# Optimization experiments

Measured on AMD Instinct MI355X. Metric: run time of the kernel, lower is better.

## Reference

```python
import jax, jax.numpy as jnp
import numpy as np
from jax.scipy.special import logsumexp

B, T, D = 16, 512, 768
S, H, O = 4, 48, 48
EMISS_W = 0.5  # args.emiss_nn_weight


def setup_inputs() -> dict:
    key = jax.random.key(0)
    ks = jax.random.split(key, 6)
    emb = jax.random.normal(ks[0], (B, T, D), jnp.float32)
    # obs must be valid per-source distributions over n_obs (log is taken)
    obs = jax.nn.softmax(2.0 * jax.random.normal(ks[1], (B, T, S, O), jnp.float32), axis=-1)
    # default prior init: priors = 0.001, priors[0] = 1, param = log(priors)
    p = jnp.full((H,), 0.001, jnp.float32).at[0].set(1.0)
    state_priors = jnp.log(p)
    unnorm_trans = jax.random.normal(ks[2], (H, H), jnp.float32)
    unnorm_emiss = jnp.zeros((S, H, O), jnp.float32)
    # xavier_uniform with relu gain for the per-source emission Linears
    bound = np.sqrt(2.0) * np.sqrt(6.0 / (D + H * O))
    W_emiss = jax.random.uniform(ks[3], (S, H * O, D), jnp.float32, -bound, bound)
    b_emiss = jnp.zeros((S, H * O), jnp.float32)
    seq_lengths = jax.random.randint(ks[4], (B,), T // 2, T + 1).astype(jnp.int32)
    seq_lengths = seq_lengths.at[0].set(T)  # max length == T
    return dict(emb=emb, obs=obs, state_priors=state_priors, unnorm_trans=unnorm_trans,
                unnorm_emiss=unnorm_emiss, W_emiss=W_emiss, b_emiss=b_emiss,
                seq_lengths=seq_lengths)


def _lognorm(x):
    return x - logsumexp(x, axis=-1, keepdims=True)


def reference(emb, obs, state_priors, unnorm_trans, unnorm_emiss, W_emiss, b_emiss, seq_lengths):
    lp = jax.nn.log_softmax(state_priors)                 # [H]
    log_trans = jax.nn.log_softmax(unnorm_trans, axis=-1)  # [H,H] (constant over b,t)
    emiss = jax.nn.softmax(unnorm_emiss, axis=-1)          # [S,H,O]

    # neural emissions: per-source Linear(d_emb -> H*O), softmax over O
    logits = jnp.einsum('btd,sod->btso', emb, W_emiss) + b_emiss  # [B,T,S,H*O]
    nn_emiss = jax.nn.softmax(logits.reshape(B, T, S, H, O), axis=-1)
    # (nn_trans is computed by NeuralModule in the original but discarded)

    log_emiss = jnp.log((1.0 - EMISS_W) * emiss[None, None] + EMISS_W * nn_emiss)  # [B,T,S,H,O]
    # log_matmul over obs axis, then sum over sources -> [B,T,H]
    lep = logsumexp(log_emiss + jnp.log(obs)[:, :, :, None, :], axis=-1).sum(axis=2)

    # forward recursion (normalized each step)
    a0 = _lognorm(lp + lep[:, 0])                          # [B,H]

    def fstep(a_prev, lep_t):
        a = _lognorm(lep_t + logsumexp(a_prev[:, :, None] + log_trans[None], axis=1))
        return a, a

    _, alphas = jax.lax.scan(fstep, a0, jnp.swapaxes(lep[:, 1:], 0, 1))
    log_alpha = jnp.concatenate([a0[:, None], jnp.swapaxes(alphas, 0, 1)], axis=1)  # [B,T,H]

    # backward recursion: beta[t] = logsumexp_j(trans[i,j] + lep[t,j] + beta[t+1,j])
    bT = jnp.zeros((B, H), lep.dtype)

    def bstep(b_next, lep_t):
        b = logsumexp(log_trans[None] + (lep_t + b_next)[:, None, :], axis=2)
        return b, b

    _, betas = jax.lax.scan(bstep, bT, jnp.swapaxes(lep[:, :T - 1], 0, 1), reverse=True)
    log_beta = jnp.concatenate([jnp.swapaxes(betas, 0, 1), bT[:, None]], axis=1)  # [B,T,H]
    # per-example roll by (length - T) along time, as in the original
    log_beta = jax.vmap(lambda b, s: jnp.roll(b, s, axis=0))(log_beta, seq_lengths - T)

    log_gamma = _lognorm(log_alpha + log_beta)             # [B,T,H]

    # xi_t = trans + alpha[t-1] (outer-sum) (lep[t] + beta[t]),  t = 1..T-1
    xi = (log_trans[None, None]
          + log_alpha[:, :-1, :, None]
          + (lep[:, 1:] + log_beta[:, 1:])[:, :, None, :])  # [B,T-1,H,H]
    xi = xi - logsumexp(xi, axis=(-2, -1), keepdims=True)

    log_prior = jnp.mean(jnp.sum(jnp.exp(log_gamma[:, 0]) * lp, axis=-1))

    tran_terms = jnp.sum(jnp.exp(xi) * log_trans[None, None], axis=(-2, -1))  # [B,T-1]
    mask_tr = (jnp.arange(T - 1)[None] < (seq_lengths - 1)[:, None]).astype(lep.dtype)
    log_tran = jnp.mean(jnp.sum(tran_terms * mask_tr, axis=1))

    emis_terms = jnp.sum(jnp.exp(log_gamma) * lep, axis=-1)  # [B,T]
    mask_em = (jnp.arange(T)[None] < seq_lengths[:, None]).astype(lep.dtype)
    log_emis = jnp.mean(jnp.sum(emis_terms * mask_em, axis=1))

    return log_prior + log_tran + log_emis
```

## Files before the change

### kernel.cpp

```cpp
#include <hip/hip_runtime.h>
#include <math.h>

namespace {

constexpr int Bn = 16, Tn = 512, Dn = 768, Sn = 4, Hn = 48, On = 48;
constexpr int Mn = Bn * Tn;
constexpr int Gn = Sn * Hn;
constexpr int Nn = Gn * On;
constexpr float EMISS_W = 0.5f;

constexpr size_t OFF_LP   = 0;
constexpr size_t OFF_LT   = 64;
constexpr size_t OFF_PT   = OFF_LT + Hn*Hn;
constexpr size_t OFF_EM   = OFF_PT + Hn*Hn;
constexpr size_t OFF_LEPP = OFF_EM + (size_t)Sn*Hn*On;
constexpr size_t OFF_LEP  = OFF_LEPP + (size_t)Mn*Gn;
constexpr size_t OFF_LA   = OFF_LEP + (size_t)Mn*Hn;
constexpr size_t OFF_LB   = OFF_LA + (size_t)Mn*Hn;
constexpr size_t OFF_RED  = OFF_LB + (size_t)Mn*Hn;
constexpr size_t FLOATS_END = OFF_RED + (size_t)Mn;

typedef __attribute__((ext_vector_type(8))) short short8;
typedef __attribute__((ext_vector_type(4))) float f32x4;

__device__ inline float waveSum(float v){
#pragma unroll
  for (int o = 32; o; o >>= 1) v += __shfl_xor(v, o);
  return v;
}

__device__ inline unsigned short f2bf(float f){
  unsigned int u = __float_as_uint(f);
  u += 0x7FFFu + ((u >> 16) & 1u);
  return (unsigned short)(u >> 16);
}

__device__ inline void gload_lds16(const void* g, void* l){
  __builtin_amdgcn_global_load_lds(
      (const __attribute__((address_space(1))) void*)g,
      (__attribute__((address_space(3))) void*)l, 16, 0, 0);
}

__global__ void conv_kernel(const float* __restrict__ srcA, unsigned short* __restrict__ dstA,
                            int n4a,
                            const float* __restrict__ srcB, unsigned short* __restrict__ dstB,
                            int n4b){
  int i = blockIdx.x * blockDim.x + threadIdx.x;
  const float* s; unsigned short* d; int k;
  if (i < n4a){ s = srcA; d = dstA; k = i; }
  else { k = i - n4a; if (k >= n4b) return; s = srcB; d = dstB; }
  float4 v = ((const float4*)s)[k];
  ushort4 r;
  r.x = f2bf(v.x); r.y = f2bf(v.y); r.z = f2bf(v.z); r.w = f2bf(v.w);
  ((ushort4*)d)[k] = r;
}

__global__ void prep_kernel(const float* __restrict__ sp, const float* __restrict__ ut,
                            const float* __restrict__ ue, float* __restrict__ ws){
  int tid = threadIdx.x;
  float m = -INFINITY;
  for (int h = 0; h < Hn; ++h) m = fmaxf(m, sp[h]);
  float s = 0.f;
  for (int h = 0; h < Hn; ++h) s += __expf(sp[h] - m);
  float lse = m + __logf(s);
  if (tid < Hn) ws[OFF_LP + tid] = sp[tid] - lse;
  if (tid < Hn){
    const float* row = ut + tid * Hn;
    float mm = -INFINITY;
    for (int j = 0; j < Hn; ++j) mm = fmaxf(mm, row[j]);
    float ss = 0.f;
    for (int j = 0; j < Hn; ++j) ss += __expf(row[j] - mm);
    float l = mm + __logf(ss);
    for (int j = 0; j < Hn; ++j){
      float v = row[j] - l;
      ws[OFF_LT + tid*Hn + j] = v;
      ws[OFF_PT + tid*Hn + j] = __expf(v);
    }
  }
  for (int r = tid; r < Sn*Hn; r += blockDim.x){
    const float* row = ue + (size_t)r * On;
    float mm = -INFINITY;
    for (int o = 0; o < On; ++o) mm = fmaxf(mm, row[o]);
    float ss = 0.f;
    for (int o = 0; o < On; ++o) ss += __expf(row[o] - mm);
    float inv = 1.f/ss;
    for (int o = 0; o < On; ++o) ws[OFF_EM + (size_t)r*On + o] = __expf(row[o]-mm)*inv;
  }
}

constexpr int MT = 128, NT2 = 96, KT = 64;

__global__ __launch_bounds__(256) void gemm_lep_kernel(
    const unsigned short* __restrict__ embB, const unsigned short* __restrict__ WB,
    const float* __restrict__ bm, const float* __restrict__ obs,
    float* __restrict__ ws){
  __shared__ __align__(16) char smem[128*97*4];
  __shared__ float bias_s[96], em_s[96];
  const int tid = threadIdx.x, lane = tid & 63, w = tid >> 6;
  const int m0 = blockIdx.x * MT;
  const int N0 = blockIdx.y * NT2;
  if (tid < 96){
    bias_s[tid] = bm[N0 + tid];
    em_s[tid]   = ws[OFF_EM + N0 + tid];
  }
  const int wm = w & 1, wn = w >> 1;
  const int lm = lane & 15, q = lane >> 4;
  const int key = lm & 7;
  const int srow = lane >> 3, spc = lane & 7;

  f32x4 acc[4][3];
#pragma unroll
  for (int i=0;i<4;++i)
#pragma unroll
    for (int j=0;j<3;++j) acc[i][j] = (f32x4){0.f,0.f,0.f,0.f};

  for (int kc = 0; kc < Dn; kc += KT){
    __syncthreads();
#pragma unroll
    for (int i=0;i<4;++i){
      int idx = w*4 + i;
      int row = idx*8 + srow;
      int lc  = spc ^ (row & 7);
      gload_lds16(embB + (size_t)(m0+row)*Dn + kc + lc*8, smem + idx*1024);
    }
#pragma unroll
    for (int i=0;i<3;++i){
      int idx = w*3 + i;
      int row = idx*8 + srow;
      int lc  = spc ^ (row & 7);
      gload_lds16(WB + (size_t)(N0+row)*Dn + kc + lc*8, smem + 16384 + idx*1024);
    }
    __syncthreads();
#pragma unroll
    for (int s = 0; s < 2; ++s){
      short8 af[4], bf[3];
#pragma unroll
      for (int i=0;i<4;++i){
        int row = wm*64 + i*16 + lm;
        af[i] = *(const short8*)(smem + row*128 + (((s*4+q) ^ key) * 16));
      }
#pragma unroll
      for (int j=0;j<3;++j){
        int row = wn*48 + j*16 + lm;
        bf[j] = *(const short8*)(smem + 16384 + row*128 + (((s*4+q) ^ key) * 16));
      }
#pragma unroll
      for (int i=0;i<4;++i)
#pragma unroll
        for (int j=0;j<3;++j)
          acc[i][j] = __builtin_amdgcn_mfma_f32_16x16x32_bf16(af[i], bf[j], acc[i][j], 0, 0, 0);
    }
  }
  __syncthreads();
  float* C = (float*)smem;
#pragma unroll
  for (int i=0;i<4;++i)
#pragma unroll
    for (int j=0;j<3;++j)
#pragma unroll
      for (int r=0;r<4;++r){
        int mrow = wm*64 + i*16 + q*4 + r;
        int ncol = wn*48 + j*16 + lm;
        C[mrow*97 + ncol] = acc[i][j][r];
      }
  __syncthreads();
  {
    const int row = tid >> 1, half = tid & 1;
    const int m = m0 + row;
    const int g = N0/48 + half;
    const int s2 = g / Hn;
    const float* crow = C + row*97 + half*48;
    const float* ob   = obs + ((size_t)m*Sn + s2)*On;
    const float* bi   = bias_s + half*48;
    const float* em   = em_s + half*48;
    float Z=0.f, pd=0.f, eo=0.f;
#pragma unroll
    for (int o=0;o<On;++o){
      float e = __expf(crow[o] + bi[o]);
      float obv = ob[o];
      Z += e;
      pd = fmaf(e, obv, pd);
      eo = fmaf(em[o], obv, eo);
    }
    float val = __logf((1.f-EMISS_W)*eo + EMISS_W*(pd/Z));
    ws[OFF_LEPP + (size_t)m*Gn + g] = val;
  }
}

__global__ void lep_reduce_kernel(float* __restrict__ ws){
  int x = blockIdx.x * blockDim.x + threadIdx.x;
  if (x < Mn*Hn){
    int m = x / Hn, h = x - m*Hn;
    const size_t base = OFF_LEPP + (size_t)m*Gn + h;
    ws[OFF_LEP + x] = ws[base] + ws[base + Hn] + ws[base + 2*Hn] + ws[base + 3*Hn];
  }
}

constexpr int FBW = 40;
constexpr int FBL = 32;

__global__ __launch_bounds__(64) void fb_kernel(float* __restrict__ ws){
  __shared__ __align__(16) float ldsE[72*48];
  __shared__ __align__(16) float ring[2][64];
  const int lane = threadIdx.x;
  const int c    = blockIdx.x;
  const int b    = blockIdx.y;
  const bool fwd = blockIdx.z == 0;
  const bool act = lane < Hn;
  const int t0 = c*FBL, te = t0 + FBL - 1;

  float pt[Hn];
#pragma unroll
  for (int i = 0; i < Hn; ++i)
    pt[i] = act ? (fwd ? ws[OFF_PT + i*Hn + lane] : ws[OFF_PT + lane*Hn + i]) : 0.f;

  int row_lo, nrows, sA, sZ;
  bool exact;
  if (fwd){
    sA = t0 - FBW;
    exact = (sA < 1);
    row_lo = exact ? 0 : sA;
    if (exact) sA = 1;
    sZ = te;
    nrows = te - row_lo + 1;
  } else {
    int th = te + 1 + FBW;
    exact = (th > 510);
    sA = exact ? 510 : th - 1;
    sZ = t0;
    row_lo = t0;
    nrows = sA - t0 + 1;
  }

  {
    const float4* src = (const float4*)(ws + OFF_LEP + ((size_t)b*Tn + row_lo)*Hn);
    int n4 = nrows * (Hn/4);
    for (int i = lane; i < n4; i += 64){
      float4 v = src[i];
      float4 e;
      e.x = __expf(v.x); e.y = __expf(v.y); e.z = __expf(v.z); e.w = __expf(v.w);
      ((float4*)ldsE)[i] = e;
    }
  }
  __syncthreads();

  if (fwd){
    const size_t laF = OFF_LA + (size_t)b * Tn * Hn;
    float v;
    if (exact){
      v = act ? __expf(ws[OFF_LP + lane]) * ldsE[lane] : 0.f;
      if (c == 0 && act) ws[laF + lane] = v;
    } else {
      v = act ? 1.f : 0.f;
    }
    if (act) ring[0][lane] = v;
    __syncthreads();
    int cur = 0;
    for (int t = sA; t <= sZ; ++t){
      float S = waveSum(v);
      const float* rp = ring[cur];
      float s0=0.f,s1=0.f,s2=0.f,s3=0.f;
#pragma unroll
      for (int i = 0; i < Hn; i += 4){
        float4 a = *(const float4*)(rp + i);
        s0 = fmaf(a.x, pt[i+0], s0); s1 = fmaf(a.y, pt[i+1], s1);
        s2 = fmaf(a.z, pt[i+2], s2); s3 = fmaf(a.w, pt[i+3], s3);
      }
      float sd = (s0+s1)+(s2+s3);
      float e = act ? ldsE[(t - row_lo)*Hn + lane] : 0.f;
      float vn = act ? e * sd * (1.f/S) : 0.f;
      cur ^= 1;
      if (act) ring[cur][lane] = vn;
      __syncthreads();
      if (act && t >= t0) ws[laF + (size_t)t*Hn + lane] = vn;
      v = vn;
    }
  } else {
    const size_t lbF = OFF_LB + (size_t)b * Tn * Hn;
    float v = act ? 1.f : 0.f;
    if (exact && c == (Tn/FBL - 1) && act) ws[lbF + (size_t)(Tn-1)*Hn + lane] = 1.f;
    int cur = 0;
    for (int t = sA; t >= sZ; --t){
      float e = act ? ldsE[(t - row_lo)*Hn + lane] : 0.f;
      float wv = e * v;
      if (act) ring[cur][lane] = wv;
      float S = waveSum(wv);
      __syncthreads();
      const float* rp = ring[cur];
      float s0=0.f,s1=0.f,s2=0.f,s3=0.f;
#pragma unroll
      for (int j = 0; j < Hn; j += 4){
        float4 a = *(const float4*)(rp + j);
        s0 = fmaf(a.x, pt[j+0], s0); s1 = fmaf(a.y, pt[j+1], s1);
        s2 = fmaf(a.z, pt[j+2], s2); s3 = fmaf(a.w, pt[j+3], s3);
      }
      float vn = act ? ((s0+s1)+(s2+s3)) * (1.f/S) : 0.f;
      cur ^= 1;
      if (act && t <= te) ws[lbF + (size_t)t*Hn + lane] = vn;
      v = vn;
    }
  }
}

__global__ __launch_bounds__(256) void gamma_xi_kernel(
    const float* __restrict__ ws_c, float* __restrict__ ws,
    const int* __restrict__ seq_len){
  __shared__ float y_s[Hn], lap_s[Hn];
  __shared__ float red[8];
  const int tid = threadIdx.x;
  const int bid = blockIdx.x;
  const int b = bid >> 9, t = bid & (Tn-1);
  const int len = seq_len[b];
  int tb = t + (Tn - len); if (tb >= Tn) tb -= Tn;
  const size_t bt = (size_t)b*Tn + t;
  if (tid < Hn){
    float lb  = ws_c[OFF_LB + ((size_t)b*Tn + tb)*Hn + tid];
    float lep = ws_c[OFF_LEP + bt*Hn + tid];
    y_s[tid] = __expf(lep) * lb;
    if (t >= 1) lap_s[tid] = ws_c[OFF_LA + (bt-1)*Hn + tid];
  }
  float emis_term = 0.f, prior_term = 0.f;
  if (tid < 64){
    int h = (tid < Hn) ? tid : 0;
    float la  = ws_c[OFF_LA + bt*Hn + h];
    float lb  = ws_c[OFF_LB + ((size_t)b*Tn + tb)*Hn + h];
    float lep = ws_c[OFF_LEP + bt*Hn + h];
    float lp  = ws_c[OFF_LP + h];
    float wgt = (tid < Hn) ? la*lb : 0.f;
    float Z = waveSum(wgt);
    float inv = 1.f / Z;
    emis_term  = waveSum(wgt * lep) * inv;
    prior_term = waveSum(wgt * lp) * inv;
  }
  __syncthreads();
  float tran_term = 0.f;
  if (t >= 1){
    float se = 0.f, st = 0.f;
#pragma unroll
    for (int k=0;k<9;++k){
      int e = tid + k*256;
      int i = e / Hn, j = e - i*Hn;
      float e2 = ws_c[OFF_PT + e] * lap_s[i] * y_s[j];
      se += e2;
      st = fmaf(e2, ws_c[OFF_LT + e], st);
    }
    se = waveSum(se);
    st = waveSum(st);
    const int wid = tid >> 6;
    if ((tid & 63) == 0){ red[wid] = se; red[4+wid] = st; }
    __syncthreads();
    if (tid == 0){
      float SE = red[0]+red[1]+red[2]+red[3];
      float ST = red[4]+red[5]+red[6]+red[7];
      tran_term = ST / SE;
    }
  }
  if (tid == 0){
    float tot = 0.f;
    if (t < len)            tot += emis_term;
    if (t == 0)             tot += prior_term;
    if (t >= 1 && t < len)  tot += tran_term;
    ws[OFF_RED + bid] = tot;
  }
}

__global__ __launch_bounds__(256) void sum_kernel(const float* __restrict__ ws,
                                                  float* __restrict__ out){
  __shared__ float red[4];
  const int tid = threadIdx.x;
  float s = 0.f;
  for (int i = tid; i < Mn; i += 256) s += ws[OFF_RED + i];
  s = waveSum(s);
  if ((tid & 63) == 0) red[tid >> 6] = s;
  __syncthreads();
  if (tid == 0) out[0] = (red[0]+red[1]+red[2]+red[3]) * (1.f / Bn);
}

}

extern "C" void kernel_launch(void* const* d_in, const int* in_sizes, int n_in,
                              void* d_out, int out_size, void* d_ws, size_t ws_size,
                              hipStream_t stream){
  const float* emb = (const float*)d_in[0];
  const float* obs = (const float*)d_in[1];
  const float* sp  = (const float*)d_in[2];
  const float* ut  = (const float*)d_in[3];
  const float* ue  = (const float*)d_in[4];
  const float* Wm  = (const float*)d_in[5];
  const float* bm  = (const float*)d_in[6];
  const int*   sl  = (const int*)d_in[7];
  float* ws  = (float*)d_ws;
  float* out = (float*)d_out;
  (void)in_sizes; (void)n_in; (void)ws_size; (void)out_size;

  unsigned short* embB = (unsigned short*)(ws + FLOATS_END);
  unsigned short* WB   = embB + (size_t)Mn * Dn;

  const int n4a = Mn*Dn/4, n4b = Nn*Dn/4;
  conv_kernel<<<(n4a + n4b + 255)/256, 256, 0, stream>>>(emb, embB, n4a, Wm, WB, n4b);
  prep_kernel<<<1, 256, 0, stream>>>(sp, ut, ue, ws);
  gemm_lep_kernel<<<dim3(Mn/MT, Nn/NT2), 256, 0, stream>>>(embB, WB, bm, obs, ws);
  lep_reduce_kernel<<<(Mn*Hn + 255)/256, 256, 0, stream>>>(ws);
  fb_kernel<<<dim3(Tn/FBL, Bn, 2), 64, 0, stream>>>(ws);
  gamma_xi_kernel<<<Bn*Tn, 256, 0, stream>>>(ws, ws, sl);
  sum_kernel<<<1, 256, 0, stream>>>(ws, out);
}
```

Baseline: 322.0 us.

## Fuse prep into conv, drop lep_reduce and sum kernels, shrink fb chunks

Merges the parameter-prep kernel into the bf16 conversion kernel as an extra block, removes the separate per-source lep reduction by summing the four partial LEPP values inside fb_kernel and gamma_xi_kernel, and replaces the final sum kernel with a last-block atomic counter reduction. It also halves the forward/backward chunk length and shortens the warm-up window, which doubles the fb block count and cuts each block's serial chain. This saves three launches and one intermediate buffer pass. In exchange the LEPP reads are repeated across consumers, and the shorter warm-up window may change numerical accuracy.

```diff
diff --git a/kernel.cpp b/kernel.cpp
--- a/kernel.cpp
+++ b/kernel.cpp
@@ -14,11 +14,11 @@
 constexpr size_t OFF_PT   = OFF_LT + Hn*Hn;
 constexpr size_t OFF_EM   = OFF_PT + Hn*Hn;
 constexpr size_t OFF_LEPP = OFF_EM + (size_t)Sn*Hn*On;
-constexpr size_t OFF_LEP  = OFF_LEPP + (size_t)Mn*Gn;
-constexpr size_t OFF_LA   = OFF_LEP + (size_t)Mn*Hn;
+constexpr size_t OFF_LA   = OFF_LEPP + (size_t)Mn*Gn;
 constexpr size_t OFF_LB   = OFF_LA + (size_t)Mn*Hn;
 constexpr size_t OFF_RED  = OFF_LB + (size_t)Mn*Hn;
-constexpr size_t FLOATS_END = OFF_RED + (size_t)Mn;
+constexpr size_t OFF_CNT  = OFF_RED + (size_t)Mn;
+constexpr size_t FLOATS_END = OFF_CNT + 64;
 
 typedef __attribute__((ext_vector_type(8))) short short8;
 typedef __attribute__((ext_vector_type(4))) float f32x4;
@@ -41,51 +41,54 @@
       (__attribute__((address_space(3))) void*)l, 16, 0, 0);
 }
 
-__global__ void conv_kernel(const float* __restrict__ srcA, unsigned short* __restrict__ dstA,
-                            int n4a,
-                            const float* __restrict__ srcB, unsigned short* __restrict__ dstB,
-                            int n4b){
-  int i = blockIdx.x * blockDim.x + threadIdx.x;
-  const float* s; unsigned short* d; int k;
-  if (i < n4a){ s = srcA; d = dstA; k = i; }
-  else { k = i - n4a; if (k >= n4b) return; s = srcB; d = dstB; }
-  float4 v = ((const float4*)s)[k];
+__global__ void convprep_kernel(const float* __restrict__ srcA, unsigned short* __restrict__ dstA,
+                                int n4a,
+                                const float* __restrict__ srcB, unsigned short* __restrict__ dstB,
+                                int n4b,
+                                const float* __restrict__ sp, const float* __restrict__ ut,
+                                const float* __restrict__ ue, float* __restrict__ ws,
+                                int nconv){
+  const int tid = threadIdx.x;
+  if ((int)blockIdx.x == nconv){
+    if (tid == 0) ((unsigned int*)(ws + OFF_CNT))[0] = 0u;
+    float m = -INFINITY;
+    for (int h = 0; h < Hn; ++h) m = fmaxf(m, sp[h]);
+    float s = 0.f;
+    for (int h = 0; h < Hn; ++h) s += __expf(sp[h] - m);
+    float lse = m + __logf(s);
+    if (tid < Hn) ws[OFF_LP + tid] = sp[tid] - lse;
+    if (tid < Hn){
+      const float* row = ut + tid * Hn;
+      float mm = -INFINITY;
+      for (int j = 0; j < Hn; ++j) mm = fmaxf(mm, row[j]);
+      float ss = 0.f;
+      for (int j = 0; j < Hn; ++j) ss += __expf(row[j] - mm);
+      float l = mm + __logf(ss);
+      for (int j = 0; j < Hn; ++j){
+        float v = row[j] - l;
+        ws[OFF_LT + tid*Hn + j] = v;
+        ws[OFF_PT + tid*Hn + j] = __expf(v);
+      }
+    }
+    for (int r = tid; r < Sn*Hn; r += blockDim.x){
+      const float* row = ue + (size_t)r * On;
+      float mm = -INFINITY;
+      for (int o = 0; o < On; ++o) mm = fmaxf(mm, row[o]);
+      float ss = 0.f;
+      for (int o = 0; o < On; ++o) ss += __expf(row[o] - mm);
+      float inv = 1.f/ss;
+      for (int o = 0; o < On; ++o) ws[OFF_EM + (size_t)r*On + o] = __expf(row[o]-mm)*inv;
+    }
+    return;
+  }
+  int i = blockIdx.x * blockDim.x + tid;
+  const float* s2; unsigned short* d; int k;
+  if (i < n4a){ s2 = srcA; d = dstA; k = i; }
+  else { k = i - n4a; if (k >= n4b) return; s2 = srcB; d = dstB; }
+  float4 v = ((const float4*)s2)[k];
   ushort4 r;
   r.x = f2bf(v.x); r.y = f2bf(v.y); r.z = f2bf(v.z); r.w = f2bf(v.w);
   ((ushort4*)d)[k] = r;
-}
-
-__global__ void prep_kernel(const float* __restrict__ sp, const float* __restrict__ ut,
-                            const float* __restrict__ ue, float* __restrict__ ws){
-  int tid = threadIdx.x;
-  float m = -INFINITY;
-  for (int h = 0; h < Hn; ++h) m = fmaxf(m, sp[h]);
-  float s = 0.f;
-  for (int h = 0; h < Hn; ++h) s += __expf(sp[h] - m);
-  float lse = m + __logf(s);
-  if (tid < Hn) ws[OFF_LP + tid] = sp[tid] - lse;
-  if (tid < Hn){
-    const float* row = ut + tid * Hn;
-    float mm = -INFINITY;
-    for (int j = 0; j < Hn; ++j) mm = fmaxf(mm, row[j]);
-    float ss = 0.f;
-    for (int j = 0; j < Hn; ++j) ss += __expf(row[j] - mm);
-    float l = mm + __logf(ss);
-    for (int j = 0; j < Hn; ++j){
-      float v = row[j] - l;
-      ws[OFF_LT + tid*Hn + j] = v;
-      ws[OFF_PT + tid*Hn + j] = __expf(v);
-    }
-  }
-  for (int r = tid; r < Sn*Hn; r += blockDim.x){
-    const float* row = ue + (size_t)r * On;
-    float mm = -INFINITY;
-    for (int o = 0; o < On; ++o) mm = fmaxf(mm, row[o]);
-    float ss = 0.f;
-    for (int o = 0; o < On; ++o) ss += __expf(row[o] - mm);
-    float inv = 1.f/ss;
-    for (int o = 0; o < On; ++o) ws[OFF_EM + (size_t)r*On + o] = __expf(row[o]-mm)*inv;
-  }
 }
 
 constexpr int MT = 128, NT2 = 96, KT = 64;
@@ -187,20 +190,11 @@
   }
 }
 
-__global__ void lep_reduce_kernel(float* __restrict__ ws){
-  int x = blockIdx.x * blockDim.x + threadIdx.x;
-  if (x < Mn*Hn){
-    int m = x / Hn, h = x - m*Hn;
-    const size_t base = OFF_LEPP + (size_t)m*Gn + h;
-    ws[OFF_LEP + x] = ws[base] + ws[base + Hn] + ws[base + 2*Hn] + ws[base + 3*Hn];
-  }
-}
-
-constexpr int FBW = 40;
-constexpr int FBL = 32;
+constexpr int FBW = 24;
+constexpr int FBL = 16;
 
 __global__ __launch_bounds__(64) void fb_kernel(float* __restrict__ ws){
-  __shared__ __align__(16) float ldsE[72*48];
+  __shared__ __align__(16) float ldsE[(FBW+FBL)*48];
   __shared__ __align__(16) float ring[2][64];
   const int lane = threadIdx.x;
   const int c    = blockIdx.x;
@@ -225,20 +219,28 @@
     nrows = te - row_lo + 1;
   } else {
     int th = te + 1 + FBW;
-    exact = (th > 510);
-    sA = exact ? 510 : th - 1;
+    exact = (th > Tn - 2);
+    sA = exact ? Tn - 2 : th - 1;
     sZ = t0;
     row_lo = t0;
     nrows = sA - t0 + 1;
   }
 
   {
-    const float4* src = (const float4*)(ws + OFF_LEP + ((size_t)b*Tn + row_lo)*Hn);
+    const float* src = ws + OFF_LEPP + ((size_t)b*Tn + row_lo)*Gn;
     int n4 = nrows * (Hn/4);
     for (int i = lane; i < n4; i += 64){
-      float4 v = src[i];
+      int r = i / (Hn/4), h4 = i - r*(Hn/4);
+      const float* p = src + (size_t)r*Gn + h4*4;
+      float4 a = *(const float4*)(p);
+      float4 b2 = *(const float4*)(p + Hn);
+      float4 c2 = *(const float4*)(p + 2*Hn);
+      float4 d2 = *(const float4*)(p + 3*Hn);
       float4 e;
-      e.x = __expf(v.x); e.y = __expf(v.y); e.z = __expf(v.z); e.w = __expf(v.w);
+      e.x = __expf(a.x + b2.x + c2.x + d2.x);
+      e.y = __expf(a.y + b2.y + c2.y + d2.y);
+      e.z = __expf(a.z + b2.z + c2.z + d2.z);
+      e.w = __expf(a.w + b2.w + c2.w + d2.w);
       ((float4*)ldsE)[i] = e;
     }
   }
@@ -304,18 +306,21 @@
 
 __global__ __launch_bounds__(256) void gamma_xi_kernel(
     const float* __restrict__ ws_c, float* __restrict__ ws,
-    const int* __restrict__ seq_len){
+    const int* __restrict__ seq_len, float* __restrict__ out){
   __shared__ float y_s[Hn], lap_s[Hn];
   __shared__ float red[8];
+  __shared__ int isLast;
   const int tid = threadIdx.x;
   const int bid = blockIdx.x;
   const int b = bid >> 9, t = bid & (Tn-1);
   const int len = seq_len[b];
   int tb = t + (Tn - len); if (tb >= Tn) tb -= Tn;
   const size_t bt = (size_t)b*Tn + t;
+  float lep = 0.f;
   if (tid < Hn){
+    const float* lpp = ws_c + OFF_LEPP + bt*Gn + tid;
+    lep = lpp[0] + lpp[Hn] + lpp[2*Hn] + lpp[3*Hn];
     float lb  = ws_c[OFF_LB + ((size_t)b*Tn + tb)*Hn + tid];
-    float lep = ws_c[OFF_LEP + bt*Hn + tid];
     y_s[tid] = __expf(lep) * lb;
     if (t >= 1) lap_s[tid] = ws_c[OFF_LA + (bt-1)*Hn + tid];
   }
@@ -324,7 +329,6 @@
     int h = (tid < Hn) ? tid : 0;
     float la  = ws_c[OFF_LA + bt*Hn + h];
     float lb  = ws_c[OFF_LB + ((size_t)b*Tn + tb)*Hn + h];
-    float lep = ws_c[OFF_LEP + bt*Hn + h];
     float lp  = ws_c[OFF_LP + h];
     float wgt = (tid < Hn) ? la*lb : 0.f;
     float Z = waveSum(wgt);
@@ -361,19 +365,20 @@
     if (t == 0)             tot += prior_term;
     if (t >= 1 && t < len)  tot += tran_term;
     ws[OFF_RED + bid] = tot;
-  }
-}
-
-__global__ __launch_bounds__(256) void sum_kernel(const float* __restrict__ ws,
-                                                  float* __restrict__ out){
-  __shared__ float red[4];
-  const int tid = threadIdx.x;
-  float s = 0.f;
-  for (int i = tid; i < Mn; i += 256) s += ws[OFF_RED + i];
-  s = waveSum(s);
-  if ((tid & 63) == 0) red[tid >> 6] = s;
+    __threadfence();
+    unsigned old = atomicAdd((unsigned*)(ws + OFF_CNT), 1u);
+    isLast = (old == (unsigned)(Mn - 1)) ? 1 : 0;
+  }
   __syncthreads();
-  if (tid == 0) out[0] = (red[0]+red[1]+red[2]+red[3]) * (1.f / Bn);
+  if (isLast){
+    __threadfence();
+    float s = 0.f;
+    for (int i = tid; i < Mn; i += 256) s += ws[OFF_RED + i];
+    s = waveSum(s);
+    if ((tid & 63) == 0) red[tid >> 6] = s;
+    __syncthreads();
+    if (tid == 0) out[0] = (red[0]+red[1]+red[2]+red[3]) * (1.f / Bn);
+  }
 }
 
 }
@@ -397,11 +402,10 @@
   unsigned short* WB   = embB + (size_t)Mn * Dn;
 
   const int n4a = Mn*Dn/4, n4b = Nn*Dn/4;
-  conv_kernel<<<(n4a + n4b + 255)/256, 256, 0, stream>>>(emb, embB, n4a, Wm, WB, n4b);
-  prep_kernel<<<1, 256, 0, stream>>>(sp, ut, ue, ws);
+  const int nconv = (n4a + n4b + 255)/256;
+  convprep_kernel<<<nconv + 1, 256, 0, stream>>>(emb, embB, n4a, Wm, WB, n4b,
+                                                 sp, ut, ue, ws, nconv);
   gemm_lep_kernel<<<dim3(Mn/MT, Nn/NT2), 256, 0, stream>>>(embB, WB, bm, obs, ws);
-  lep_reduce_kernel<<<(Mn*Hn + 255)/256, 256, 0, stream>>>(ws);
   fb_kernel<<<dim3(Tn/FBL, Bn, 2), 64, 0, stream>>>(ws);
-  gamma_xi_kernel<<<Bn*Tn, 256, 0, stream>>>(ws, ws, sl);
-  sum_kernel<<<1, 256, 0, stream>>>(ws, out);
-}
+  gamma_xi_kernel<<<Bn*Tn, 256, 0, stream>>>(ws, ws, sl, out);
+}
```

New measurement: 437.1 us. 35.7% more time.
